# Kernel optimization log

Hardware: AMD Instinct MI355X
Metric: run time of the kernel (lower is better)

The kernel has to match this reference:

```python
import jax, jax.numpy as jnp
import numpy as np

B, LQ, LKV, D = 16, 2048, 2048, 64
MASK_VALUE = -1000000.0


def setup_inputs() -> dict:
    key = jax.random.key(0)
    kq, kk, kv, kl = jax.random.split(key, 4)
    queries = jax.random.normal(kq, (B, LQ, D), dtype=jnp.float32)
    keys = jax.random.normal(kk, (B, LKV, D), dtype=jnp.float32)
    values = jax.random.normal(kv, (B, LKV, D), dtype=jnp.float32)
    valid_lens = jax.random.randint(kl, (B,), 1, LKV + 1, dtype=jnp.int32)
    return {"queries": queries, "keys": keys, "values": values, "valid_lens": valid_lens}


def reference(queries, keys, values, valid_lens):
    d = queries.shape[-1]
    # scores: [B, Lq, Lkv]
    scores = jnp.einsum('bqd,bkd->bqk', queries, keys) / jnp.sqrt(jnp.float32(d))
    # valid_lens is per-batch; positions >= valid_len are masked to -1e6 (not -inf),
    # matching torch masked_fill semantics before softmax.
    col = jnp.arange(scores.shape[-1], dtype=jnp.int32)            # [Lkv]
    mask = col[None, None, :] >= valid_lens[:, None, None]          # [B, 1, Lkv] -> broadcast over Lq
    scores = jnp.where(mask, jnp.float32(MASK_VALUE), scores)
    attn = jax.nn.softmax(scores, axis=-1)
    # dropout p=0.0 (eval) -> identity
    return jnp.einsum('bqk,bkd->bqd', attn, values)
```

## Files before the change

### kernel.cpp

```cpp
#include <hip/hip_runtime.h>
#include <hip/hip_bf16.h>


#define NB   16
#define LQS  2048
#define LKVS 2048
#define DH   64
#define QBLK 64
#define KVB  64

typedef short bf16x8 __attribute__((ext_vector_type(8)));
typedef float f32x4  __attribute__((ext_vector_type(4)));

__device__ __forceinline__ unsigned short f2bf(float x) {
    return __builtin_bit_cast(unsigned short, __float2bfloat16(x));
}
__device__ __forceinline__ float bf2f(unsigned short h) {
    return __uint_as_float(((unsigned int)h) << 16);
}
__device__ __forceinline__ int vswz(int d) {
    return (((d & 7) ^ (d >> 3)) << 3);
}

__global__ __launch_bounds__(512, 4) void attn_fa(
    const float* __restrict__ Qg, const float* __restrict__ Kg,
    const float* __restrict__ Vg, const int* __restrict__ vlg,
    float* __restrict__ Og)
{
    __shared__ __align__(16) unsigned short sMem[2][4 * KVB * DH];

    const int b    = blockIdx.y;
    const int q0   = blockIdx.x * QBLK;
    const int tid  = threadIdx.x;
    const int wg   = tid >> 8;
    const int gtid = tid & 255;
    const int w4   = (tid >> 6) & 3;
    const int lane = tid & 63;
    const int lr   = lane & 15;
    const int lg   = lane >> 4;
    const int n_valid = vlg[b];

    unsigned short* sKhi = &sMem[wg][0];
    unsigned short* sKlo = &sMem[wg][4096];
    unsigned short* sVhi = &sMem[wg][8192];
    unsigned short* sVlo = &sMem[wg][12288];

    const int kb = (gtid >> 4) * 4;
    const int db = (gtid & 15) * 4;
    const int pb = (kb & ~31) | (((kb >> 2) & 3) << 3) | (((kb >> 4) & 1) << 2);

    bf16x8 qhi[2], qlo[2];
    {
        const float* qp = Qg + ((size_t)b * LQS + q0 + w4 * 16 + lr) * DH;
        #pragma unroll
        for (int s = 0; s < 2; ++s) {
            const float4 a = *(const float4*)(qp + s * 32 + lg * 8);
            const float4 c = *(const float4*)(qp + s * 32 + lg * 8 + 4);
            const float vv[8] = {a.x, a.y, a.z, a.w, c.x, c.y, c.z, c.w};
            #pragma unroll
            for (int i = 0; i < 8; ++i) {
                const float x = vv[i] * 0.125f;
                const unsigned short h = f2bf(x);
                qhi[s][i] = (short)h;
                qlo[s][i] = (short)f2bf(x - bf2f(h));
            }
        }
    }

    f32x4 o[4];
    #pragma unroll
    for (int nt = 0; nt < 4; ++nt) { o[nt][0]=0.f; o[nt][1]=0.f; o[nt][2]=0.f; o[nt][3]=0.f; }
    float m_q = -__builtin_inff();
    float l_q = 0.f;

    const int nsteps = (n_valid + KVB - 1) / KVB;
    const int rounds = (nsteps + 1) >> 1;

    float4 kq[4], vr[4];
    if (wg < nsteps) {
        const float* kp = Kg + ((size_t)b * LKVS + wg * KVB) * DH;
        const float* vp = Vg + ((size_t)b * LKVS + wg * KVB) * DH;
        #pragma unroll
        for (int it = 0; it < 4; ++it) {
            const int idx = gtid + it * 256;
            kq[it] = *(const float4*)(kp + (idx >> 4) * DH + (idx & 15) * 4);
        }
        #pragma unroll
        for (int j = 0; j < 4; ++j)
            vr[j] = *(const float4*)(vp + (kb + j) * DH + db);
    }

    for (int jt = 0; jt < rounds; ++jt) {
        const int st  = 2 * jt + wg;
        const bool act = (st < nsteps);
        const int kv0 = st * KVB;
        __syncthreads();
        if (act) {
            #pragma unroll
            for (int it = 0; it < 4; ++it) {
                const int idx = gtid + it * 256;
                const int key = idx >> 4, f4 = idx & 15;
                const float ka[4] = {kq[it].x, kq[it].y, kq[it].z, kq[it].w};
                unsigned short kh[4], kl[4];
                #pragma unroll
                for (int i = 0; i < 4; ++i) {
                    kh[i] = f2bf(ka[i]);
                    kl[i] = f2bf(ka[i] - bf2f(kh[i]));
                }
                const int kb_ = key * 64 + (((f4 * 4) & ~7) ^ ((key & 7) << 3)) + (f4 & 1) * 4;
                *(ushort4*)(&sKhi[kb_]) = make_ushort4(kh[0], kh[1], kh[2], kh[3]);
                *(ushort4*)(&sKlo[kb_]) = make_ushort4(kl[0], kl[1], kl[2], kl[3]);
            }
            #pragma unroll
            for (int i = 0; i < 4; ++i) {
                const int d = db + i;
                const float f0 = (&vr[0].x)[i], f1 = (&vr[1].x)[i];
                const float f2_ = (&vr[2].x)[i], f3 = (&vr[3].x)[i];
                const unsigned short h0 = f2bf(f0), h1 = f2bf(f1);
                const unsigned short h2 = f2bf(f2_), h3 = f2bf(f3);
                const int vi = d * 64 + (pb ^ vswz(d));
                *(ushort4*)(&sVhi[vi]) = make_ushort4(h0, h1, h2, h3);
                *(ushort4*)(&sVlo[vi]) = make_ushort4(
                    f2bf(f0 - bf2f(h0)), f2bf(f1 - bf2f(h1)),
                    f2bf(f2_ - bf2f(h2)), f2bf(f3 - bf2f(h3)));
            }
        }
        __syncthreads();

        {
            const int stn = st + 2;
            if (stn < nsteps) {
                const float* kp = Kg + ((size_t)b * LKVS + stn * KVB) * DH;
                const float* vp = Vg + ((size_t)b * LKVS + stn * KVB) * DH;
                #pragma unroll
                for (int it = 0; it < 4; ++it) {
                    const int idx = gtid + it * 256;
                    kq[it] = *(const float4*)(kp + (idx >> 4) * DH + (idx & 15) * 4);
                }
                #pragma unroll
                for (int j = 0; j < 4; ++j)
                    vr[j] = *(const float4*)(vp + (kb + j) * DH + db);
            }
        }

        if (act) {
            float p_[4][4];
            __builtin_amdgcn_s_setprio(1);
            #pragma unroll
            for (int kt = 0; kt < 4; ++kt) {
                f32x4 acc = {0.f, 0.f, 0.f, 0.f};
                const int key = kt * 16 + lr;
                #pragma unroll
                for (int s = 0; s < 2; ++s) {
                    const int ki = key * 64 + ((s * 32 + lg * 8) ^ ((key & 7) << 3));
                    const bf16x8 khi = *(const bf16x8*)(&sKhi[ki]);
                    const bf16x8 klo = *(const bf16x8*)(&sKlo[ki]);
                    acc = __builtin_amdgcn_mfma_f32_16x16x32_bf16(khi, qhi[s], acc, 0, 0, 0);
                    acc = __builtin_amdgcn_mfma_f32_16x16x32_bf16(khi, qlo[s], acc, 0, 0, 0);
                    acc = __builtin_amdgcn_mfma_f32_16x16x32_bf16(klo, qhi[s], acc, 0, 0, 0);
                }
                #pragma unroll
                for (int r = 0; r < 4; ++r) p_[kt][r] = acc[r];
            }
            __builtin_amdgcn_s_setprio(0);

            if (kv0 + KVB > n_valid) {
                #pragma unroll
                for (int kt = 0; kt < 4; ++kt) {
                    #pragma unroll
                    for (int r = 0; r < 4; ++r) {
                        if (kv0 + kt * 16 + lg * 4 + r >= n_valid) p_[kt][r] = -1000000.0f;
                    }
                }
            }

            float tm = p_[0][0];
            #pragma unroll
            for (int kt = 0; kt < 4; ++kt) {
                #pragma unroll
                for (int r = 0; r < 4; ++r) tm = fmaxf(tm, p_[kt][r]);
            }
            tm = fmaxf(tm, __shfl_xor(tm, 16));
            tm = fmaxf(tm, __shfl_xor(tm, 32));
            const float mn = fmaxf(m_q, tm);
            const float sc = __expf(m_q - mn);
            float rs = 0.f;
            #pragma unroll
            for (int kt = 0; kt < 4; ++kt) {
                #pragma unroll
                for (int r = 0; r < 4; ++r) {
                    p_[kt][r] = __expf(p_[kt][r] - mn);
                    rs += p_[kt][r];
                }
            }
            rs += __shfl_xor(rs, 16);
            rs += __shfl_xor(rs, 32);
            l_q = l_q * sc + rs;
            m_q = mn;
            #pragma unroll
            for (int r = 0; r < 4; ++r) {
                const float scr = __shfl(sc, lg * 4 + r);
                #pragma unroll
                for (int nt = 0; nt < 4; ++nt) o[nt][r] *= scr;
            }

            #pragma unroll
            for (int s = 0; s < 2; ++s) {
                bf16x8 phi, plo;
                #pragma unroll
                for (int i = 0; i < 8; ++i) {
                    const float v = p_[2 * s + (i >> 2)][i & 3];
                    const unsigned short h = f2bf(v);
                    phi[i] = (short)h;
                    plo[i] = (short)f2bf(v - bf2f(h));
                }
                const int cb = s * 32 + lg * 8;
                __builtin_amdgcn_s_setprio(1);
                #pragma unroll
                for (int nt = 0; nt < 4; ++nt) {
                    const int d  = nt * 16 + lr;
                    const int vi = d * 64 + (cb ^ vswz(d));
                    const bf16x8 vhi = *(const bf16x8*)(&sVhi[vi]);
                    const bf16x8 vlo = *(const bf16x8*)(&sVlo[vi]);
                    o[nt] = __builtin_amdgcn_mfma_f32_16x16x32_bf16(phi, vhi, o[nt], 0, 0, 0);
                    o[nt] = __builtin_amdgcn_mfma_f32_16x16x32_bf16(plo, vhi, o[nt], 0, 0, 0);
                    o[nt] = __builtin_amdgcn_mfma_f32_16x16x32_bf16(phi, vlo, o[nt], 0, 0, 0);
                }
                __builtin_amdgcn_s_setprio(0);
            }
        }
    }

    __syncthreads();
    float* fo = (float*)&sMem[0][0];
    if (wg == 1) {
        #pragma unroll
        for (int nt = 0; nt < 4; ++nt) {
            #pragma unroll
            for (int r = 0; r < 4; ++r)
                fo[(nt * 4 + r) * 256 + w4 * 64 + lane] = o[nt][r];
        }
        if (lg == 0) {
            fo[4096 + w4 * 16 + lr] = m_q;
            fo[4160 + w4 * 16 + lr] = l_q;
        }
    }
    __syncthreads();
    if (wg == 0) {
        const float m1 = fo[4096 + w4 * 16 + lr];
        const float l1 = fo[4160 + w4 * 16 + lr];
        const float mm = fmaxf(m_q, m1);
        const float a0 = __expf(m_q - mm);
        const float a1 = __expf(m1 - mm);
        const float inv = 1.0f / (a0 * l_q + a1 * l1);
        #pragma unroll
        for (int r = 0; r < 4; ++r) {
            const float a0r  = __shfl(a0, lg * 4 + r);
            const float a1r  = __shfl(a1, lg * 4 + r);
            const float invr = __shfl(inv, lg * 4 + r);
            const int row = lg * 4 + r;
            float* op = Og + ((size_t)b * LQS + q0 + w4 * 16 + row) * DH + lr;
            #pragma unroll
            for (int nt = 0; nt < 4; ++nt) {
                const float o1 = fo[(nt * 4 + r) * 256 + w4 * 64 + lane];
                op[nt * 16] = (a0r * o[nt][r] + a1r * o1) * invr;
            }
        }
    }
}

extern "C" void kernel_launch(void* const* d_in, const int* in_sizes, int n_in,
                              void* d_out, int out_size, void* d_ws, size_t ws_size,
                              hipStream_t stream) {
    (void)in_sizes; (void)n_in; (void)out_size; (void)d_ws; (void)ws_size;
    const float* Q  = (const float*)d_in[0];
    const float* K  = (const float*)d_in[1];
    const float* V  = (const float*)d_in[2];
    const int*   vl = (const int*)d_in[3];
    float* O = (float*)d_out;
    dim3 grid(LQS / QBLK, NB);
    attn_fa<<<grid, 512, 0, stream>>>(Q, K, V, vl, O);
}
```

Baseline: 119.6 us.

## Split KV range across grid z with workspace partials and a combine kernel

Adds a split-KV flash attention kernel that divides each batch's valid KV tiles into four chunks of eight tiles along grid z, with 128-query blocks of eight waves. Each block writes unnormalized partial outputs plus row max and sum to the workspace, and a second kernel merges them. This targets the load imbalance that comes from varying valid lengths across the batch and uses more blocks to fill the GPU. In exchange it adds workspace traffic (four partial output tensors) and a second launch, and it falls back to the old kernel when the workspace is too small.

```diff
diff --git a/kernel.cpp b/kernel.cpp
--- a/kernel.cpp
+++ b/kernel.cpp
@@ -6,8 +6,9 @@
 #define LQS  2048
 #define LKVS 2048
 #define DH   64
-#define QBLK 64
 #define KVB  64
+#define NZ   4
+#define TPZ  8
 
 typedef short bf16x8 __attribute__((ext_vector_type(8)));
 typedef float f32x4  __attribute__((ext_vector_type(4)));
@@ -20,6 +21,241 @@
 }
 __device__ __forceinline__ int vswz(int d) {
     return (((d & 7) ^ (d >> 3)) << 3);
+}
+
+__global__ __launch_bounds__(512, 8) void attn_fa_split(
+    const float* __restrict__ Qg, const float* __restrict__ Kg,
+    const float* __restrict__ Vg, const int* __restrict__ vlg,
+    float* __restrict__ Po, float* __restrict__ Pm, float* __restrict__ Pl)
+{
+    __shared__ __align__(16) unsigned short sKhi[KVB * DH];
+    __shared__ __align__(16) unsigned short sKlo[KVB * DH];
+    __shared__ __align__(16) unsigned short sVhi[DH * KVB];
+    __shared__ __align__(16) unsigned short sVlo[DH * KVB];
+
+    const int b    = blockIdx.y;
+    const int z    = blockIdx.z;
+    const int q0   = blockIdx.x * 128;
+    const int tid  = threadIdx.x;
+    const int w8   = tid >> 6;
+    const int lane = tid & 63;
+    const int lr   = lane & 15;
+    const int lg   = lane >> 4;
+    const int n_valid = vlg[b];
+
+    const int nsteps  = (n_valid + KVB - 1) / KVB;
+    const int t_begin = z * TPZ;
+    const int t_end   = min(nsteps, t_begin + TPZ);
+    const int ntiles  = max(0, t_end - t_begin);
+
+    const int kb2 = ((tid >> 4) & 31) * 2;
+    const int db  = (tid & 15) * 4;
+    const int pos2 = (kb2 & 32) | (((kb2 >> 2) & 3) << 3) | (((kb2 >> 4) & 1) << 2) | (kb2 & 3);
+
+    bf16x8 qhi[2], qlo[2];
+    {
+        const float* qp = Qg + ((size_t)b * LQS + q0 + w8 * 16 + lr) * DH;
+        #pragma unroll
+        for (int s = 0; s < 2; ++s) {
+            const float4 a = *(const float4*)(qp + s * 32 + lg * 8);
+            const float4 c = *(const float4*)(qp + s * 32 + lg * 8 + 4);
+            const float vv[8] = {a.x, a.y, a.z, a.w, c.x, c.y, c.z, c.w};
+            #pragma unroll
+            for (int i = 0; i < 8; ++i) {
+                const float x = vv[i] * 0.125f;
+                const unsigned short h = f2bf(x);
+                qhi[s][i] = (short)h;
+                qlo[s][i] = (short)f2bf(x - bf2f(h));
+            }
+        }
+    }
+
+    f32x4 o[4];
+    #pragma unroll
+    for (int nt = 0; nt < 4; ++nt) { o[nt][0]=0.f; o[nt][1]=0.f; o[nt][2]=0.f; o[nt][3]=0.f; }
+    float m_q = -__builtin_inff();
+    float l_q = 0.f;
+
+    float4 kq[2], vr[2];
+    if (ntiles > 0) {
+        const float* kp = Kg + ((size_t)b * LKVS + t_begin * KVB) * DH;
+        const float* vp = Vg + ((size_t)b * LKVS + t_begin * KVB) * DH;
+        #pragma unroll
+        for (int it = 0; it < 2; ++it) {
+            const int idx = tid + it * 512;
+            kq[it] = *(const float4*)(kp + (idx >> 4) * DH + (idx & 15) * 4);
+        }
+        #pragma unroll
+        for (int j = 0; j < 2; ++j)
+            vr[j] = *(const float4*)(vp + (kb2 + j) * DH + db);
+    }
+
+    for (int stl = 0; stl < ntiles; ++stl) {
+        const int kv0 = (t_begin + stl) * KVB;
+        __syncthreads();
+        #pragma unroll
+        for (int it = 0; it < 2; ++it) {
+            const int idx = tid + it * 512;
+            const int key = idx >> 4, f4 = idx & 15;
+            const float ka[4] = {kq[it].x, kq[it].y, kq[it].z, kq[it].w};
+            unsigned short kh[4], kl[4];
+            #pragma unroll
+            for (int i = 0; i < 4; ++i) {
+                kh[i] = f2bf(ka[i]);
+                kl[i] = f2bf(ka[i] - bf2f(kh[i]));
+            }
+            const int kb_ = key * 64 + (((f4 * 4) & ~7) ^ ((key & 7) << 3)) + (f4 & 1) * 4;
+            *(ushort4*)(&sKhi[kb_]) = make_ushort4(kh[0], kh[1], kh[2], kh[3]);
+            *(ushort4*)(&sKlo[kb_]) = make_ushort4(kl[0], kl[1], kl[2], kl[3]);
+        }
+        #pragma unroll
+        for (int i = 0; i < 4; ++i) {
+            const int d = db + i;
+            const float f0 = (&vr[0].x)[i], f1 = (&vr[1].x)[i];
+            const unsigned short h0 = f2bf(f0), h1 = f2bf(f1);
+            const int vi = d * 64 + (pos2 ^ vswz(d));
+            *(ushort2*)(&sVhi[vi]) = make_ushort2(h0, h1);
+            *(ushort2*)(&sVlo[vi]) = make_ushort2(f2bf(f0 - bf2f(h0)), f2bf(f1 - bf2f(h1)));
+        }
+        __syncthreads();
+
+        if (stl + 1 < ntiles) {
+            const float* kp = Kg + ((size_t)b * LKVS + (kv0 + KVB)) * DH;
+            const float* vp = Vg + ((size_t)b * LKVS + (kv0 + KVB)) * DH;
+            #pragma unroll
+            for (int it = 0; it < 2; ++it) {
+                const int idx = tid + it * 512;
+                kq[it] = *(const float4*)(kp + (idx >> 4) * DH + (idx & 15) * 4);
+            }
+            #pragma unroll
+            for (int j = 0; j < 2; ++j)
+                vr[j] = *(const float4*)(vp + (kb2 + j) * DH + db);
+        }
+
+        float p_[4][4];
+        __builtin_amdgcn_s_setprio(1);
+        #pragma unroll
+        for (int kt = 0; kt < 4; ++kt) {
+            f32x4 acc = {0.f, 0.f, 0.f, 0.f};
+            const int key = kt * 16 + lr;
+            #pragma unroll
+            for (int s = 0; s < 2; ++s) {
+                const int ki = key * 64 + ((s * 32 + lg * 8) ^ ((key & 7) << 3));
+                const bf16x8 khi = *(const bf16x8*)(&sKhi[ki]);
+                const bf16x8 klo = *(const bf16x8*)(&sKlo[ki]);
+                acc = __builtin_amdgcn_mfma_f32_16x16x32_bf16(khi, qhi[s], acc, 0, 0, 0);
+                acc = __builtin_amdgcn_mfma_f32_16x16x32_bf16(khi, qlo[s], acc, 0, 0, 0);
+                acc = __builtin_amdgcn_mfma_f32_16x16x32_bf16(klo, qhi[s], acc, 0, 0, 0);
+            }
+            #pragma unroll
+            for (int r = 0; r < 4; ++r) p_[kt][r] = acc[r];
+        }
+        __builtin_amdgcn_s_setprio(0);
+
+        if (kv0 + KVB > n_valid) {
+            #pragma unroll
+            for (int kt = 0; kt < 4; ++kt) {
+                #pragma unroll
+                for (int r = 0; r < 4; ++r) {
+                    if (kv0 + kt * 16 + lg * 4 + r >= n_valid) p_[kt][r] = -1000000.0f;
+                }
+            }
+        }
+
+        float tm = p_[0][0];
+        #pragma unroll
+        for (int kt = 0; kt < 4; ++kt) {
+            #pragma unroll
+            for (int r = 0; r < 4; ++r) tm = fmaxf(tm, p_[kt][r]);
+        }
+        tm = fmaxf(tm, __shfl_xor(tm, 16));
+        tm = fmaxf(tm, __shfl_xor(tm, 32));
+        const float mn = fmaxf(m_q, tm);
+        const float sc = __expf(m_q - mn);
+        float rs = 0.f;
+        #pragma unroll
+        for (int kt = 0; kt < 4; ++kt) {
+            #pragma unroll
+            for (int r = 0; r < 4; ++r) {
+                p_[kt][r] = __expf(p_[kt][r] - mn);
+                rs += p_[kt][r];
+            }
+        }
+        rs += __shfl_xor(rs, 16);
+        rs += __shfl_xor(rs, 32);
+        l_q = l_q * sc + rs;
+        m_q = mn;
+        #pragma unroll
+        for (int r = 0; r < 4; ++r) {
+            const float scr = __shfl(sc, lg * 4 + r);
+            #pragma unroll
+            for (int nt = 0; nt < 4; ++nt) o[nt][r] *= scr;
+        }
+
+        #pragma unroll
+        for (int s = 0; s < 2; ++s) {
+            bf16x8 phi, plo;
+            #pragma unroll
+            for (int i = 0; i < 8; ++i) {
+                const float v = p_[2 * s + (i >> 2)][i & 3];
+                const unsigned short h = f2bf(v);
+                phi[i] = (short)h;
+                plo[i] = (short)f2bf(v - bf2f(h));
+            }
+            const int cb = s * 32 + lg * 8;
+            __builtin_amdgcn_s_setprio(1);
+            #pragma unroll
+            for (int nt = 0; nt < 4; ++nt) {
+                const int d  = nt * 16 + lr;
+                const int vi = d * 64 + (cb ^ vswz(d));
+                const bf16x8 vhi = *(const bf16x8*)(&sVhi[vi]);
+                const bf16x8 vlo = *(const bf16x8*)(&sVlo[vi]);
+                o[nt] = __builtin_amdgcn_mfma_f32_16x16x32_bf16(phi, vhi, o[nt], 0, 0, 0);
+                o[nt] = __builtin_amdgcn_mfma_f32_16x16x32_bf16(plo, vhi, o[nt], 0, 0, 0);
+                o[nt] = __builtin_amdgcn_mfma_f32_16x16x32_bf16(phi, vlo, o[nt], 0, 0, 0);
+            }
+            __builtin_amdgcn_s_setprio(0);
+        }
+    }
+
+    const size_t rb = (size_t)(z * NB + b) * LQS + q0 + w8 * 16;
+    #pragma unroll
+    for (int r = 0; r < 4; ++r) {
+        const int row = lg * 4 + r;
+        float* op = Po + (rb + row) * DH + lr;
+        #pragma unroll
+        for (int nt = 0; nt < 4; ++nt) op[nt * 16] = o[nt][r];
+    }
+    if (lg == 0) {
+        Pm[rb + lr] = m_q;
+        Pl[rb + lr] = l_q;
+    }
+}
+
+__global__ __launch_bounds__(256) void attn_combine(
+    const float* __restrict__ Po, const float* __restrict__ Pm,
+    const float* __restrict__ Pl, float* __restrict__ Og)
+{
+    const int e   = blockIdx.x * 256 + threadIdx.x;
+    const int row = e >> 6;
+    float mz[NZ], lz[NZ];
+    float m = -__builtin_inff();
+    #pragma unroll
+    for (int zi = 0; zi < NZ; ++zi) {
+        mz[zi] = Pm[zi * (NB * LQS) + row];
+        lz[zi] = Pl[zi * (NB * LQS) + row];
+        m = fmaxf(m, mz[zi]);
+    }
+    float num = 0.f, den = 0.f;
+    #pragma unroll
+    for (int zi = 0; zi < NZ; ++zi) {
+        if (lz[zi] > 0.f) {
+            const float a = __expf(mz[zi] - m);
+            num += a * Po[(size_t)zi * (NB * LQS * DH) + e];
+            den += a * lz[zi];
+        }
+    }
+    Og[e] = num / den;
 }
 
 __global__ __launch_bounds__(512, 4) void attn_fa(
@@ -30,7 +266,7 @@
     __shared__ __align__(16) unsigned short sMem[2][4 * KVB * DH];
 
     const int b    = blockIdx.y;
-    const int q0   = blockIdx.x * QBLK;
+    const int q0   = blockIdx.x * 64;
     const int tid  = threadIdx.x;
     const int wg   = tid >> 8;
     const int gtid = tid & 255;
@@ -251,7 +487,7 @@
         const float l1 = fo[4160 + w4 * 16 + lr];
         const float mm = fmaxf(m_q, m1);
         const float a0 = __expf(m_q - mm);
-        const float a1 = __expf(m1 - mm);
+        const float a1 = (l1 > 0.f) ? __expf(m1 - mm) : 0.f;
         const float inv = 1.0f / (a0 * l_q + a1 * l1);
         #pragma unroll
         for (int r = 0; r < 4; ++r) {
@@ -272,12 +508,23 @@
 extern "C" void kernel_launch(void* const* d_in, const int* in_sizes, int n_in,
                               void* d_out, int out_size, void* d_ws, size_t ws_size,
                               hipStream_t stream) {
-    (void)in_sizes; (void)n_in; (void)out_size; (void)d_ws; (void)ws_size;
+    (void)in_sizes; (void)n_in; (void)out_size;
     const float* Q  = (const float*)d_in[0];
     const float* K  = (const float*)d_in[1];
     const float* V  = (const float*)d_in[2];
     const int*   vl = (const int*)d_in[3];
     float* O = (float*)d_out;
-    dim3 grid(LQS / QBLK, NB);
-    attn_fa<<<grid, 512, 0, stream>>>(Q, K, V, vl, O);
-}
+
+    const size_t oelems = (size_t)NZ * NB * LQS * DH;
+    const size_t melems = (size_t)NZ * NB * LQS;
+    const size_t need   = (oelems + 2 * melems) * sizeof(float);
+    if (ws_size >= need) {
+        float* Po = (float*)d_ws;
+        float* Pm = Po + oelems;
+        float* Pl = Pm + melems;
+        attn_fa_split<<<dim3(LQS / 128, NB, NZ), 512, 0, stream>>>(Q, K, V, vl, Po, Pm, Pl);
+        attn_combine<<<(NB * LQS * DH) / 256, 256, 0, stream>>>(Po, Pm, Pl, O);
+    } else {
+        attn_fa<<<dim3(LQS / 64, NB), 512, 0, stream>>>(Q, K, V, vl, O);
+    }
+}
```

Result: slower. 224.2 us (+87.5%).
